# Optimization experiments

Hardware: AMD Instinct MI355X
Metric: run time of the kernel (lower is better)

## Reference

```python
import jax, jax.numpy as jnp
import numpy as np


def _conv(x, w, b=None, pad=0):
    y = jax.lax.conv_general_dilated(
        x, w, window_strides=(1, 1), padding=[(pad, pad), (pad, pad)],
        dimension_numbers=('NCHW', 'OIHW', 'NCHW'))
    if b is not None:
        y = y + b[None, :, None, None]
    return y


def _resblock(x, w1, w2):
    r = _conv(x, w1, pad=1)
    r = jnp.where(r > 0, r, 0.1 * r)  # LeakyReLU(0.1)
    r = _conv(r, w2, pad=1)
    return r + x


def setup_inputs() -> dict:
    key = jax.random.key(0)
    ks = jax.random.split(key, 8)
    b, c, h, w = 8, 64, 128, 320
    return {
        'x_left': jax.random.normal(ks[0], (b, c, h, w), jnp.float32),
        'x_right': jax.random.normal(ks[1], (b, c, h, w), jnp.float32),
        'rb_w1': jax.random.normal(ks[2], (c, c, 3, 3), jnp.float32) * 0.05,
        'rb_w2': jax.random.normal(ks[3], (c, c, 3, 3), jnp.float32) * 0.05,
        'wl': jax.random.normal(ks[4], (c, c, 1, 1), jnp.float32) * 0.1,
        'bl': jax.random.normal(ks[5], (c,), jnp.float32) * 0.01,
        'wr': jax.random.normal(ks[6], (c, c, 1, 1), jnp.float32) * 0.1,
        'br': jax.random.normal(ks[7], (c,), jnp.float32) * 0.01,
    }


def reference(x_left, x_right, rb_w1, rb_w2, wl, bl, wr, br):
    b, c, h, w = x_left.shape
    buf_l = _resblock(x_left, rb_w1, rb_w2)
    buf_r = _resblock(x_right, rb_w1, rb_w2)
    # 1x1 projections, then per-row attention along width
    F0 = _conv(buf_l, wl, bl).transpose(0, 2, 3, 1)   # (b,h,w,c)
    F1 = _conv(buf_r, wr, br).transpose(0, 2, 3, 1)   # (b,h,w,c)
    S = jnp.einsum('bhwc,bhvc->bhwv', F0, F1)          # (b,h,w,w)
    M_right_to_left = jax.nn.softmax(S, axis=-1)       # (b,h,w,w)
    M_left_to_right = jax.nn.softmax(jnp.swapaxes(S, -1, -2), axis=-1)
    # validity mask: column-sum > 0.1 (detached). skimage morphology (CPU-side) is
    # intentionally omitted; it is outside the GPU kernel scope.
    V = (jnp.sum(jax.lax.stop_gradient(M_left_to_right), axis=2) > 0.1)
    V = V.reshape(b, 1, h, w).astype(jnp.float32)
    # warp right features to left view
    xr = x_right.transpose(0, 2, 3, 1)                 # (b,h,w,c)
    out_f = jnp.einsum('bhwv,bhvc->bhwc', M_right_to_left, xr)
    out_f = out_f.transpose(0, 3, 1, 2)                # (b,c,h,w)
    return (out_f, V,
            (M_left_to_right.reshape(b * h, w, w),
             M_right_to_left.reshape(b * h, w, w)))
```

## Files before the change

kernel.cpp:

```cpp
#include <hip/hip_runtime.h>

#define BB 8
#define CC 64
#define HH 128
#define WW 320

#define N_OUTF (BB*CC*HH*WW)
#define N_V    (BB*HH*WW)
#define N_M    (BB*HH*WW*WW)
#define OFF_V    (N_OUTF)
#define OFF_ML2R (N_OUTF + N_V)
#define OFF_MR2L (OFF_ML2R + N_M)
#define OUT_TOTAL (OFF_MR2L + N_M)
#define WT_FLOATS ((4*36864 + 4*4096)/2)
#define NCL 20971520
#define INV512 (1.f/512.f)

typedef _Float16 half8 __attribute__((ext_vector_type(8)));
typedef _Float16 half4 __attribute__((ext_vector_type(4)));
typedef float f32x4 __attribute__((ext_vector_type(4)));

__global__ __launch_bounds__(256) void k_wt(
    const float* __restrict__ w1, const float* __restrict__ w2,
    const float* __restrict__ wl, const float* __restrict__ wr,
    _Float16* __restrict__ wB1h, _Float16* __restrict__ wB1l,
    _Float16* __restrict__ wB2h, _Float16* __restrict__ wB2l,
    _Float16* __restrict__ wl1h, _Float16* __restrict__ wl1l,
    _Float16* __restrict__ wr1h, _Float16* __restrict__ wr1l)
{
    int tid = blockIdx.x * 256 + threadIdx.x;
    int stride = gridDim.x * 256;
    for (int e = tid; e < 64*9*64; e += stride) {
        int co = e / 576;
        int rem = e - co*576;
        int tap = rem >> 6, ci = rem & 63;
        float v1 = w1[(co*64 + ci)*9 + tap];
        float v2 = w2[(co*64 + ci)*9 + tap];
        _Float16 h1 = (_Float16)v1, h2 = (_Float16)v2;
        wB1h[e] = h1; wB1l[e] = (_Float16)((v1 - (float)h1)*512.f);
        wB2h[e] = h2; wB2l[e] = (_Float16)((v2 - (float)h2)*512.f);
    }
    for (int e = tid; e < 4096; e += stride) {
        float vl = wl[e], vr = wr[e];
        _Float16 hl = (_Float16)vl, hr = (_Float16)vr;
        wl1h[e] = hl; wl1l[e] = (_Float16)((vl - (float)hl)*512.f);
        wr1h[e] = hr; wr1l[e] = (_Float16)((vr - (float)hr)*512.f);
    }
}

__global__ __launch_bounds__(256) void k_conv_a(
    const float* __restrict__ in_l_, const float* __restrict__ in_r_,
    const _Float16* __restrict__ wBh, const _Float16* __restrict__ wBl,
    _Float16* __restrict__ r_lh, _Float16* __restrict__ r_ll,
    _Float16* __restrict__ r_rh, _Float16* __restrict__ r_rl)
{
    __shared__ __align__(16) char smem[2*4*34*128];
    char* in_sh = smem;
    char* in_sl = smem + 17408;
    const int tid = threadIdx.x;
    const int x0 = blockIdx.x * 32;
    const int y0 = blockIdx.y * 2;
    const int z  = blockIdx.z;
    const int side = z >> 3, b = z & 7;
    const float* in = side ? in_r_ : in_l_;
    _Float16* out_h = side ? r_rh : r_lh;
    _Float16* out_l = side ? r_rl : r_ll;
    const int lane = tid & 63;
    const int xq = lane & 15, kq = lane >> 4;
    const int n = tid >> 6;

    half8 bwh[18], bwl[18];
    {
        const _Float16* wbh = &wBh[((size_t)(n*16 + xq)*9)*64 + kq*8];
        const _Float16* wbl = &wBl[((size_t)(n*16 + xq)*9)*64 + kq*8];
#pragma unroll
        for (int t = 0; t < 9; ++t)
#pragma unroll
            for (int c = 0; c < 2; ++c) {
                bwh[t*2 + c] = *(const half8*)&wbh[t*64 + c*32];
                bwl[t*2 + c] = *(const half8*)&wbl[t*64 + c*32];
            }
    }

    for (int e = tid; e < 1088; e += 256) {
        int t = e / 34;
        int xx = e - t*34;
        int ry = t >> 3, u = t & 7;
        int gy = y0 + ry - 1, gx = x0 + xx - 1;
        half8 hh, hl;
#pragma unroll
        for (int j = 0; j < 8; ++j) { hh[j] = (_Float16)0.f; hl[j] = (_Float16)0.f; }
        if ((unsigned)gy < (unsigned)HH && (unsigned)gx < (unsigned)WW) {
            const float* p = &in[((size_t)(b*CC + u*8)*HH + gy)*WW + gx];
#pragma unroll
            for (int j = 0; j < 8; ++j) {
                float v = p[(size_t)j*HH*WW];
                _Float16 h = (_Float16)v;
                hh[j] = h; hl[j] = (_Float16)((v - (float)h)*512.f);
            }
        }
        int off = ((ry*34 + xx)*8 + (u ^ (xx & 7)))*16;
        *(half8*)&in_sh[off] = hh;
        *(half8*)&in_sl[off] = hl;
    }
    __syncthreads();

    f32x4 accm[2][2], accc[2][2];
#pragma unroll
    for (int rr = 0; rr < 2; ++rr)
#pragma unroll
        for (int m = 0; m < 2; ++m) { accm[rr][m] = (f32x4)0.f; accc[rr][m] = (f32x4)0.f; }

#pragma unroll
    for (int rr = 0; rr < 2; ++rr) {
#pragma unroll
        for (int m = 0; m < 2; ++m) {
            const int xb = m*16 + xq;
#pragma unroll
            for (int t = 0; t < 9; ++t) {
                const int ry = t / 3, kx = t - ry*3;
                const int trow = rr + ry;
                const int xxx = xb + kx;
#pragma unroll
                for (int c = 0; c < 2; ++c) {
                    const int u = c*4 + kq;
                    int off = ((trow*34 + xxx)*8 + (u ^ (xxx & 7)))*16;
                    half8 ah = *(const half8*)&in_sh[off];
                    half8 al = *(const half8*)&in_sl[off];
                    accm[rr][m] = __builtin_amdgcn_mfma_f32_16x16x32_f16(
                        ah, bwh[t*2 + c], accm[rr][m], 0, 0, 0);
                    accc[rr][m] = __builtin_amdgcn_mfma_f32_16x16x32_f16(
                        al, bwh[t*2 + c], accc[rr][m], 0, 0, 0);
                    accc[rr][m] = __builtin_amdgcn_mfma_f32_16x16x32_f16(
                        ah, bwl[t*2 + c], accc[rr][m], 0, 0, 0);
                }
            }
        }
    }
    __syncthreads();

    char* out_sh = smem;
    char* out_sl = smem + 8192;
#pragma unroll
    for (int rr = 0; rr < 2; ++rr) {
#pragma unroll
        for (int m = 0; m < 2; ++m) {
#pragma unroll
            for (int r = 0; r < 4; ++r) {
                int x = m*16 + kq*4 + r;
                int co = n*16 + xq;
                float v = accm[rr][m][r] + accc[rr][m][r]*INV512;
                v = (v > 0.f) ? v : 0.1f*v;
                _Float16 vh = (_Float16)v;
                _Float16 vl = (_Float16)((v - (float)vh)*512.f);
                int boff = ((rr*32 + x)*8 + ((co >> 3) ^ (x & 7)))*16 + (co & 7)*2;
                *(_Float16*)&out_sh[boff] = vh;
                *(_Float16*)&out_sl[boff] = vl;
            }
        }
    }
    __syncthreads();

#pragma unroll
    for (int i = 0; i < 2; ++i) {
        int unit = tid + 256*i;
        int rr = unit >> 8, x = (unit >> 3) & 31, u = unit & 7;
        int loff = ((rr*32 + x)*8 + (u ^ (x & 7)))*16;
        size_t g = (((size_t)(b*HH + y0 + rr)*WW) + x0 + x)*64 + u*8;
        *(half8*)&out_h[g] = *(half8*)&out_sh[loff];
        *(half8*)&out_l[g] = *(half8*)&out_sl[loff];
    }
}

__global__ __launch_bounds__(256) void k_conv_b(
    const _Float16* __restrict__ r_lh, const _Float16* __restrict__ r_ll,
    const _Float16* __restrict__ r_rh, const _Float16* __restrict__ r_rl,
    const _Float16* __restrict__ wBh, const _Float16* __restrict__ wBl,
    const float* __restrict__ res_l, const float* __restrict__ res_r,
    const _Float16* __restrict__ wl1h, const _Float16* __restrict__ wl1l,
    const _Float16* __restrict__ wr1h, const _Float16* __restrict__ wr1l,
    const float* __restrict__ bias_l, const float* __restrict__ bias_r,
    _Float16* __restrict__ F0h, _Float16* __restrict__ F0l,
    _Float16* __restrict__ F1h, _Float16* __restrict__ F1l)
{
    __shared__ __align__(16) char smem[49152];
    char* in_sh = smem;
    char* in_sl = smem + 17408;
    const int tid = threadIdx.x;
    const int x0 = blockIdx.x * 32;
    const int y0 = blockIdx.y * 2;
    const int z  = blockIdx.z;
    const int side = z >> 3, b = z & 7;
    const _Float16* in_h = side ? r_rh : r_lh;
    const _Float16* in_l = side ? r_rl : r_ll;
    const float* res = side ? res_r : res_l;
    const _Float16* w1h = side ? wr1h : wl1h;
    const _Float16* w1l = side ? wr1l : wl1l;
    const float* bias = side ? bias_r : bias_l;
    _Float16* Fh = side ? F1h : F0h;
    _Float16* Fl = side ? F1l : F0l;
    const int lane = tid & 63;
    const int xq = lane & 15, kq = lane >> 4;
    const int n = tid >> 6;

    half8 bwh[18], bwl[18];
    {
        const _Float16* wbh = &wBh[((size_t)(n*16 + xq)*9)*64 + kq*8];
        const _Float16* wbl = &wBl[((size_t)(n*16 + xq)*9)*64 + kq*8];
#pragma unroll
        for (int t = 0; t < 9; ++t)
#pragma unroll
            for (int c = 0; c < 2; ++c) {
                bwh[t*2 + c] = *(const half8*)&wbh[t*64 + c*32];
                bwl[t*2 + c] = *(const half8*)&wbl[t*64 + c*32];
            }
    }

    for (int e = tid; e < 1088; e += 256) {
        int t = e / 34;
        int xx = e - t*34;
        int ry = t >> 3, u = t & 7;
        int gy = y0 + ry - 1, gx = x0 + xx - 1;
        uint4 vh = make_uint4(0u,0u,0u,0u), vl = make_uint4(0u,0u,0u,0u);
        if ((unsigned)gy < (unsigned)HH && (unsigned)gx < (unsigned)WW) {
            size_t g = (((size_t)(b*HH + gy)*WW) + gx)*64 + u*8;
            vh = *(const uint4*)&in_h[g];
            vl = *(const uint4*)&in_l[g];
        }
        int off = ((ry*34 + xx)*8 + (u ^ (xx & 7)))*16;
        *(uint4*)&in_sh[off] = vh;
        *(uint4*)&in_sl[off] = vl;
    }
    __syncthreads();

    f32x4 accm[2][2], accc[2][2];
#pragma unroll
    for (int rr = 0; rr < 2; ++rr)
#pragma unroll
        for (int m = 0; m < 2; ++m) { accm[rr][m] = (f32x4)0.f; accc[rr][m] = (f32x4)0.f; }

#pragma unroll
    for (int rr = 0; rr < 2; ++rr) {
#pragma unroll
        for (int m = 0; m < 2; ++m) {
            const int xb = m*16 + xq;
#pragma unroll
            for (int t = 0; t < 9; ++t) {
                const int ry = t / 3, kx = t - ry*3;
                const int trow = rr + ry;
                const int xxx = xb + kx;
#pragma unroll
                for (int c = 0; c < 2; ++c) {
                    const int u = c*4 + kq;
                    int off = ((trow*34 + xxx)*8 + (u ^ (xxx & 7)))*16;
                    half8 ah = *(const half8*)&in_sh[off];
                    half8 al = *(const half8*)&in_sl[off];
                    accm[rr][m] = __builtin_amdgcn_mfma_f32_16x16x32_f16(
                        ah, bwh[t*2 + c], accm[rr][m], 0, 0, 0);
                    accc[rr][m] = __builtin_amdgcn_mfma_f32_16x16x32_f16(
                        al, bwh[t*2 + c], accc[rr][m], 0, 0, 0);
                    accc[rr][m] = __builtin_amdgcn_mfma_f32_16x16x32_f16(
                        ah, bwl[t*2 + c], accc[rr][m], 0, 0, 0);
                }
            }
        }
    }
    __syncthreads();

    char* out_sh = smem;
    char* out_sl = smem + 8192;
    char* res_sh = smem + 16384;
    char* res_sl = smem + 24576;
    char* w_sh   = smem + 32768;
    char* w_sl   = smem + 40960;

#pragma unroll
    for (int i = 0; i < 2; ++i) {
        int e = tid + 256*i;
        int rr = e >> 8, x = (e >> 3) & 31, cu = e & 7;
        const float* p = &res[((size_t)(b*CC + cu*8)*HH + y0 + rr)*WW + x0 + x];
        half8 hh, hl;
#pragma unroll
        for (int j = 0; j < 8; ++j) {
            float v = p[(size_t)j*HH*WW];
            _Float16 h = (_Float16)v;
            hh[j] = h; hl[j] = (_Float16)((v - (float)h)*512.f);
        }
        int off = ((rr*32 + x)*8 + (cu ^ (x & 7)))*16;
        *(half8*)&res_sh[off] = hh;
        *(half8*)&res_sl[off] = hl;
    }
#pragma unroll
    for (int i = 0; i < 2; ++i) {
        int e = tid + 256*i;
        int co = e >> 3, u = e & 7;
        int off = (co*8 + (u ^ (co & 7)))*16;
        *(half8*)&w_sh[off] = *(const half8*)&w1h[co*64 + u*8];
        *(half8*)&w_sl[off] = *(const half8*)&w1l[co*64 + u*8];
    }
#pragma unroll
    for (int rr = 0; rr < 2; ++rr) {
#pragma unroll
        for (int m = 0; m < 2; ++m) {
#pragma unroll
            for (int r = 0; r < 4; ++r) {
                int x = m*16 + kq*4 + r;
                int co = n*16 + xq;
                float v = accm[rr][m][r] + accc[rr][m][r]*INV512;
                _Float16 vh = (_Float16)v;
                _Float16 vl = (_Float16)((v - (float)vh)*512.f);
                int boff = ((rr*32 + x)*8 + ((co >> 3) ^ (x & 7)))*16 + (co & 7)*2;
                *(_Float16*)&out_sh[boff] = vh;
                *(_Float16*)&out_sl[boff] = vl;
            }
        }
    }
    __syncthreads();

    float bv[4];
#pragma unroll
    for (int nn = 0; nn < 4; ++nn) bv[nn] = bias[nn*16 + (lane & 15)];

    f32x4 am[4], ac[4];
#pragma unroll
    for (int nn = 0; nn < 4; ++nn) { am[nn] = (f32x4)0.f; ac[nn] = (f32x4)0.f; }

    const int arow = n*16 + (lane & 15);
#pragma unroll
    for (int c = 0; c < 4; ++c) {
        half8 ah, al;
        int u = (c & 1)*4 + (lane >> 4);
        int off = (arow*8 + (u ^ (arow & 7)))*16;
        if (c < 2) {
            ah = *(const half8*)&out_sh[off];
            al = *(const half8*)&out_sl[off];
        } else {
            ah = *(const half8*)&res_sh[off];
            al = *(const half8*)&res_sl[off];
        }
#pragma unroll
        for (int nn = 0; nn < 4; ++nn) {
            int brow = nn*16 + (lane & 15);
            int woff = (brow*8 + (u ^ (brow & 7)))*16;
            half8 bh  = *(const half8*)&w_sh[woff];
            half8 blw = *(const half8*)&w_sl[woff];
            am[nn] = __builtin_amdgcn_mfma_f32_16x16x32_f16(ah, bh,  am[nn], 0,0,0);
            ac[nn] = __builtin_amdgcn_mfma_f32_16x16x32_f16(al, bh,  ac[nn], 0,0,0);
            ac[nn] = __builtin_amdgcn_mfma_f32_16x16x32_f16(ah, blw, ac[nn], 0,0,0);
        }
    }
    __syncthreads();

    char* F_sh = smem + 16384;
    char* F_sl = smem + 24576;
#pragma unroll
    for (int nn = 0; nn < 4; ++nn) {
#pragma unroll
        for (int r = 0; r < 4; ++r) {
            int pos = n*16 + (lane >> 4)*4 + r;
            int co = nn*16 + (lane & 15);
            float v = am[nn][r] + ac[nn][r]*INV512 + bv[nn];
            _Float16 vh = (_Float16)v;
            _Float16 vl = (_Float16)((v - (float)vh)*512.f);
            int boff = (pos*8 + ((co >> 3) ^ (pos & 7)))*16 + (co & 7)*2;
            *(_Float16*)&F_sh[boff] = vh;
            *(_Float16*)&F_sl[boff] = vl;
        }
    }
    __syncthreads();

#pragma unroll
    for (int i = 0; i < 2; ++i) {
        int unit = tid + 256*i;
        int rr = unit >> 8, x = (unit >> 3) & 31, u = unit & 7;
        int loff = ((rr*32 + x)*8 + (u ^ (x & 7)))*16;
        size_t g = (((size_t)(b*HH + y0 + rr)*WW) + x0 + x)*64 + u*8;
        *(half8*)&Fh[g] = *(half8*)&F_sh[loff];
        *(half8*)&Fl[g] = *(half8*)&F_sl[loff];
    }
}

__global__ __launch_bounds__(256) void k_sgemm(
    const _Float16* __restrict__ F0h, const _Float16* __restrict__ F0l,
    const _Float16* __restrict__ F1h, const _Float16* __restrict__ F1l,
    float* __restrict__ S,
    float* __restrict__ colmax_p, float* __restrict__ colsum_p,
    float* __restrict__ rowmax_f, float* __restrict__ rowinv_f)
{
    __shared__ __align__(16) char smem[32768];
    __shared__ float cpm[2][4][64], cpl[2][4][64];
    const int wt = blockIdx.x, row = blockIdx.y;
    const int tid = threadIdx.x, lane = tid & 63, wid = tid >> 6;
    char* R0 = smem;
    char* R1 = smem + 16384;

    for (int e = tid; e < 512; e += 256) {
        int i = e >> 3, u = e & 7;
        int off = (i*8 + (u ^ (i & 7)))*16;
        size_t ga = ((size_t)row*WW + wt*64 + i)*64 + u*8;
        *(uint4*)&R0[off]        = *(const uint4*)&F0h[ga];
        *(uint4*)&R0[8192 + off] = *(const uint4*)&F0l[ga];
        size_t gb = ((size_t)row*WW + i)*64 + u*8;
        *(uint4*)&R1[off]        = *(const uint4*)&F1h[gb];
        *(uint4*)&R1[8192 + off] = *(const uint4*)&F1l[gb];
    }
    __syncthreads();

    half8 ah[2], al[2];
    {
        const int arow = wid*16 + (lane & 15);
#pragma unroll
        for (int c = 0; c < 2; ++c) {
            int u = c*4 + (lane >> 4);
            int aoff = (arow*8 + (u ^ (arow & 7)))*16;
            ah[c] = *(const half8*)&R0[aoff];
            al[c] = *(const half8*)&R0[8192 + aoff];
        }
    }

    float rm[4], rl[4];
#pragma unroll
    for (int r = 0; r < 4; ++r) { rm[r] = -1e30f; rl[r] = 0.f; }

    for (int vt = 0; vt < 5; ++vt) {
        char* cur = (vt & 1) ? R0 : R1;
        __syncthreads();
        if (vt < 4) {
            char* nxt = (vt & 1) ? R1 : R0;
            for (int e = tid; e < 512; e += 256) {
                int i = e >> 3, u = e & 7;
                int off = (i*8 + (u ^ (i & 7)))*16;
                size_t gb = ((size_t)row*WW + (vt+1)*64 + i)*64 + u*8;
                *(uint4*)&nxt[off]        = *(const uint4*)&F1h[gb];
                *(uint4*)&nxt[8192 + off] = *(const uint4*)&F1l[gb];
            }
        }
        if (vt > 0 && tid < 64) {
            int pb = (vt-1) & 1;
            float m0 = cpm[pb][0][tid], m1 = cpm[pb][1][tid];
            float m2 = cpm[pb][2][tid], m3 = cpm[pb][3][tid];
            float m = fmaxf(fmaxf(m0, m1), fmaxf(m2, m3));
            float l = cpl[pb][0][tid]*__expf(m0-m) + cpl[pb][1][tid]*__expf(m1-m)
                    + cpl[pb][2][tid]*__expf(m2-m) + cpl[pb][3][tid]*__expf(m3-m);
            size_t cbase = ((size_t)row*5 + wt)*WW + (size_t)(vt-1)*64 + tid;
            colmax_p[cbase] = m;
            colsum_p[cbase] = l;
        }

        f32x4 accm[4], accc[4];
#pragma unroll
        for (int n = 0; n < 4; ++n) { accm[n] = (f32x4)0.f; accc[n] = (f32x4)0.f; }
#pragma unroll
        for (int c = 0; c < 2; ++c) {
            const int u = c*4 + (lane >> 4);
#pragma unroll
            for (int n = 0; n < 4; ++n) {
                const int brow = n*16 + (lane & 15);
                int boff = (brow*8 + (u ^ (brow & 7)))*16;
                half8 bh = *(const half8*)&cur[boff];
                half8 bl = *(const half8*)&cur[8192 + boff];
                accm[n] = __builtin_amdgcn_mfma_f32_16x16x32_f16(ah[c], bh, accm[n], 0,0,0);
                accc[n] = __builtin_amdgcn_mfma_f32_16x16x32_f16(al[c], bh, accc[n], 0,0,0);
                accc[n] = __builtin_amdgcn_mfma_f32_16x16x32_f16(ah[c], bl, accc[n], 0,0,0);
            }
        }

        float sv[4][4];
#pragma unroll
        for (int n = 0; n < 4; ++n)
#pragma unroll
            for (int r = 0; r < 4; ++r)
                sv[n][r] = accm[n][r] + accc[n][r]*INV512;

#pragma unroll
        for (int n = 0; n < 4; ++n) {
            float* sp = &S[((size_t)row*WW + wt*64 + wid*16 + (lane>>4)*4)*WW
                           + vt*64 + n*16 + (lane & 15)];
#pragma unroll
            for (int r = 0; r < 4; ++r) sp[(size_t)r*WW] = sv[n][r];
        }

#pragma unroll
        for (int r = 0; r < 4; ++r) {
            float tmax = fmaxf(fmaxf(sv[0][r], sv[1][r]), fmaxf(sv[2][r], sv[3][r]));
            float newm = fmaxf(rm[r], tmax);
            rl[r] = rl[r]*__expf(rm[r] - newm)
                  + __expf(sv[0][r]-newm) + __expf(sv[1][r]-newm)
                  + __expf(sv[2][r]-newm) + __expf(sv[3][r]-newm);
            rm[r] = newm;
        }

#pragma unroll
        for (int n = 0; n < 4; ++n) {
            float m = fmaxf(fmaxf(sv[n][0], sv[n][1]), fmaxf(sv[n][2], sv[n][3]));
            m = fmaxf(m, __shfl_xor(m, 16));
            m = fmaxf(m, __shfl_xor(m, 32));
            float l = __expf(sv[n][0]-m) + __expf(sv[n][1]-m)
                    + __expf(sv[n][2]-m) + __expf(sv[n][3]-m);
            l += __shfl_xor(l, 16); l += __shfl_xor(l, 32);
            if (lane < 16) { cpm[vt&1][wid][n*16 + lane] = m;
                             cpl[vt&1][wid][n*16 + lane] = l; }
        }
    }
    __syncthreads();
    if (tid < 64) {
        float m0 = cpm[0][0][tid], m1 = cpm[0][1][tid];
        float m2 = cpm[0][2][tid], m3 = cpm[0][3][tid];
        float m = fmaxf(fmaxf(m0, m1), fmaxf(m2, m3));
        float l = cpl[0][0][tid]*__expf(m0-m) + cpl[0][1][tid]*__expf(m1-m)
                + cpl[0][2][tid]*__expf(m2-m) + cpl[0][3][tid]*__expf(m3-m);
        size_t cbase = ((size_t)row*5 + wt)*WW + 4*64 + tid;
        colmax_p[cbase] = m;
        colsum_p[cbase] = l;
    }

#pragma unroll
    for (int r = 0; r < 4; ++r) {
#pragma unroll
        for (int o = 1; o < 16; o <<= 1) {
            float m2 = __shfl_xor(rm[r], o);
            float l2 = __shfl_xor(rl[r], o);
            float mm = fmaxf(rm[r], m2);
            rl[r] = rl[r]*__expf(rm[r] - mm) + l2*__expf(m2 - mm);
            rm[r] = mm;
        }
    }
    if ((lane & 15) == 0) {
        size_t rbase = (size_t)row*WW + wt*64 + wid*16 + (lane>>4)*4;
#pragma unroll
        for (int r = 0; r < 4; ++r) {
            rowmax_f[rbase + r] = rm[r];
            rowinv_f[rbase + r] = 1.f / rl[r];
        }
    }
}

__global__ __launch_bounds__(320) void k_smerge(
    const float* __restrict__ colmax_p, const float* __restrict__ colsum_p,
    float* __restrict__ colmax_f, float* __restrict__ colinv_f)
{
    const int row = blockIdx.x, tid = threadIdx.x;
    float m = -1e30f, l = 0.f;
#pragma unroll
    for (int t = 0; t < 5; ++t) {
        float pm = colmax_p[((size_t)row*5 + t)*WW + tid];
        float pl = colsum_p[((size_t)row*5 + t)*WW + tid];
        float m2 = fmaxf(m, pm);
        l = l*__expf(m - m2) + pl*__expf(pm - m2);
        m = m2;
    }
    colmax_f[(size_t)row*WW + tid] = m;
    colinv_f[(size_t)row*WW + tid] = 1.f/l;
}

__global__ __launch_bounds__(256) void k_fused(
    float* __restrict__ S, float* __restrict__ Ml2r, float* __restrict__ Vout,
    const float* __restrict__ xr, float* __restrict__ outf,
    const float* __restrict__ colmax_f, const float* __restrict__ colinv_f,
    const float* __restrict__ rowmax_f, const float* __restrict__ rowinv_f)
{
    __shared__ __align__(16) char A[8192], Bm[8192];
    __shared__ float T[64*65];
    __shared__ float cmx[320], cin[320], rmx[64], rin[64];
    const int wt = blockIdx.x, row = blockIdx.y;
    const int b = row >> 7, h = row & 127;
    const int tid = threadIdx.x, lane = tid & 63, wid = tid >> 6;
    const int wrow = tid >> 2, quad = tid & 3;

    for (int e = tid; e < 320; e += 256) {
        cmx[e] = colmax_f[(size_t)row*WW + e];
        cin[e] = colinv_f[(size_t)row*WW + e];
    }
    if (tid < 64) {
        rmx[tid] = rowmax_f[(size_t)row*WW + wt*64 + tid];
        rin[tid] = rowinv_f[(size_t)row*WW + wt*64 + tid];
    }
    __syncthreads();

    f32x4 acc[4];
#pragma unroll
    for (int n = 0; n < 4; ++n) acc[n] = (f32x4)0.f;
    float vsum = 0.f;
    float* Sbase = &S[((size_t)row*WW + wt*64 + wrow)*WW];
    const float rm = rmx[wrow], ri = rin[wrow];

    float4 s_pre[4];
#pragma unroll
    for (int i = 0; i < 4; ++i)
        s_pre[i] = *(float4*)&Sbase[(quad + 4*i)*4];

    for (int vt = 0; vt < 5; ++vt) {
        if (vt) __syncthreads();
        float4 s_cur[4];
#pragma unroll
        for (int i = 0; i < 4; ++i) s_cur[i] = s_pre[i];
        if (vt < 4) {
#pragma unroll
            for (int i = 0; i < 4; ++i)
                s_pre[i] = *(float4*)&Sbase[(vt+1)*64 + (quad + 4*i)*4];
        }
#pragma unroll
        for (int i = 0; i < 4; ++i) {
            const int f = quad + 4*i;
            const int v0 = f*4;
            float4 s = s_cur[i];
            float4 pr;
            pr.x = __expf(s.x - rm)*ri;
            pr.y = __expf(s.y - rm)*ri;
            pr.z = __expf(s.z - rm)*ri;
            pr.w = __expf(s.w - rm)*ri;
            *(float4*)&Sbase[vt*64 + v0] = pr;
            const int vg = vt*64 + v0;
            float p0 = __expf(s.x - cmx[vg+0])*cin[vg+0];
            float p1 = __expf(s.y - cmx[vg+1])*cin[vg+1];
            float p2 = __expf(s.z - cmx[vg+2])*cin[vg+2];
            float p3 = __expf(s.w - cmx[vg+3])*cin[vg+3];
            T[(v0+0)*65 + wrow] = p0;
            T[(v0+1)*65 + wrow] = p1;
            T[(v0+2)*65 + wrow] = p2;
            T[(v0+3)*65 + wrow] = p3;
            vsum += p0 + p1 + p2 + p3;
            half4 hp;
            hp[0] = (_Float16)pr.x; hp[1] = (_Float16)pr.y;
            hp[2] = (_Float16)pr.z; hp[3] = (_Float16)pr.w;
            *(half4*)&A[(wrow*8 + ((f>>1) ^ (wrow & 7)))*16 + (f & 1)*8] = hp;
        }
        for (int e = tid; e < 512; e += 256) {
            int i = e >> 3, u = e & 7;
            const float4* xp = (const float4*)
                &xr[(((size_t)b*CC + i)*HH + h)*WW + vt*64 + u*8];
            float4 b0 = xp[0], b1 = xp[1];
            half8 hb;
            hb[0]=(_Float16)b0.x; hb[1]=(_Float16)b0.y; hb[2]=(_Float16)b0.z;
            hb[3]=(_Float16)b0.w; hb[4]=(_Float16)b1.x; hb[5]=(_Float16)b1.y;
            hb[6]=(_Float16)b1.z; hb[7]=(_Float16)b1.w;
            *(half8*)&Bm[(i*8 + (u ^ (i & 7)))*16] = hb;
        }
        __syncthreads();
#pragma unroll
        for (int c = 0; c < 2; ++c) {
            const int u = c*4 + (lane >> 4);
            const int arow = wid*16 + (lane & 15);
            half8 ah = *(const half8*)&A[(arow*8 + (u ^ (arow & 7)))*16];
#pragma unroll
            for (int n = 0; n < 4; ++n) {
                const int brow = n*16 + (lane & 15);
                half8 bh = *(const half8*)&Bm[(brow*8 + (u ^ (brow & 7)))*16];
                acc[n] = __builtin_amdgcn_mfma_f32_16x16x32_f16(ah, bh, acc[n], 0,0,0);
            }
        }
        for (int e = tid; e < 1024; e += 256) {
            int vr = e >> 4, wc4 = (e & 15)*4;
            const float* tp = &T[vr*65 + wc4];
            *(float4*)&Ml2r[((size_t)row*WW + vt*64 + vr)*WW + wt*64 + wc4] =
                make_float4(tp[0], tp[1], tp[2], tp[3]);
        }
    }

    vsum += __shfl_xor(vsum, 1);
    vsum += __shfl_xor(vsum, 2);
    if (quad == 0)
        Vout[(size_t)row*WW + wt*64 + wrow] = (vsum > 0.1f) ? 1.f : 0.f;

#pragma unroll
    for (int n = 0; n < 4; ++n) {
        *(float4*)&outf[(((size_t)b*CC + n*16 + (lane & 15))*HH + h)*WW
                        + wt*64 + wid*16 + (lane>>4)*4] =
            make_float4(acc[n][0], acc[n][1], acc[n][2], acc[n][3]);
    }
}

__global__ __launch_bounds__(320) void k_softmax(
    float* __restrict__ S, float* __restrict__ Ml2r, float* __restrict__ Vout,
    const float* __restrict__ colmax_f, const float* __restrict__ colinv_f,
    const float* __restrict__ rowmax_f, const float* __restrict__ rowinv_f)
{
    __shared__ float rowmax[320], rowinv[320], colmax[320], colinv[320];
    __shared__ float T[64*65];
    __shared__ float Vp2[5*64];
    const int row = blockIdx.x;
    const int tid = threadIdx.x;
    float* Srow = &S[(size_t)row * WW * WW];

    rowmax[tid] = rowmax_f[(size_t)row*WW + tid];
    rowinv[tid] = rowinv_f[(size_t)row*WW + tid];
    colmax[tid] = colmax_f[(size_t)row*WW + tid];
    colinv[tid] = colinv_f[(size_t)row*WW + tid];
    __syncthreads();

    const int myw = tid & 63;
    const int myg = tid / 64;
    for (int wt = 0; wt < 5; ++wt) {
        float vpart = 0.f;
        for (int vt = 0; vt < 5; ++vt) {
            for (int e = tid; e < 4096; e += 320) {
                int i = e >> 6, j = e & 63;
                int wgl = wt*64 + i, vgl = vt*64 + j;
                size_t si = (size_t)wgl*WW + vgl;
                float s = Srow[si];
                Srow[si] = __expf(s - rowmax[wgl]) * rowinv[wgl];
                T[j*65 + i] = __expf(s - colmax[vgl]) * colinv[vgl];
            }
            __syncthreads();
            for (int e = tid; e < 4096; e += 320) {
                int vr = e >> 6, wc = e & 63;
                Ml2r[((size_t)row*WW + vt*64 + vr)*WW + wt*64 + wc] = T[vr*65 + wc];
            }
            for (int j = myg; j < 64; j += 5) vpart += T[j*65 + myw];
            __syncthreads();
        }
        Vp2[myg*64 + myw] = vpart;
        __syncthreads();
        if (tid < 64) {
            float sv = 0.f;
#pragma unroll
            for (int g = 0; g < 5; ++g) sv += Vp2[g*64 + tid];
            Vout[(size_t)row*WW + wt*64 + tid] = (sv > 0.1f) ? 1.f : 0.f;
        }
        __syncthreads();
    }
}

__global__ __launch_bounds__(256) void k_outgemm(
    const float* __restrict__ M, const float* __restrict__ xr,
    float* __restrict__ outf)
{
    __shared__ __align__(16) char Am[8192], Bm[8192];
    const int wt = blockIdx.x;
    const int row = blockIdx.y;
    const int b = row >> 7, h = row & 127;
    const int tid = threadIdx.x, lane = tid & 63, wid = tid >> 6;

    f32x4 acc[4];
#pragma unroll
    for (int n = 0; n < 4; ++n) acc[n] = (f32x4)0.f;

    for (int vt = 0; vt < 5; ++vt) {
        if (vt) __syncthreads();
        for (int e = tid; e < 512; e += 256) {
            int i = e >> 3, u = e & 7;
            const float4* mp = (const float4*)
                &M[((size_t)row*WW + wt*64 + i)*WW + vt*64 + u*8];
            float4 a0 = mp[0], a1 = mp[1];
            const float4* xp = (const float4*)
                &xr[(((size_t)b*CC + i)*HH + h)*WW + vt*64 + u*8];
            float4 b0 = xp[0], b1 = xp[1];
            half8 ha, hb;
            ha[0]=(_Float16)a0.x; ha[1]=(_Float16)a0.y; ha[2]=(_Float16)a0.z;
            ha[3]=(_Float16)a0.w; ha[4]=(_Float16)a1.x; ha[5]=(_Float16)a1.y;
            ha[6]=(_Float16)a1.z; ha[7]=(_Float16)a1.w;
            hb[0]=(_Float16)b0.x; hb[1]=(_Float16)b0.y; hb[2]=(_Float16)b0.z;
            hb[3]=(_Float16)b0.w; hb[4]=(_Float16)b1.x; hb[5]=(_Float16)b1.y;
            hb[6]=(_Float16)b1.z; hb[7]=(_Float16)b1.w;
            int off = (i*8 + (u ^ (i & 7)))*16;
            *(half8*)&Am[off] = ha;
            *(half8*)&Bm[off] = hb;
        }
        __syncthreads();
#pragma unroll
        for (int c = 0; c < 2; ++c) {
            const int u = c*4 + (lane >> 4);
            const int arow = wid*16 + (lane & 15);
            half8 ah = *(const half8*)&Am[(arow*8 + (u ^ (arow & 7)))*16];
#pragma unroll
            for (int n = 0; n < 4; ++n) {
                const int brow = n*16 + (lane & 15);
                half8 bh = *(const half8*)&Bm[(brow*8 + (u ^ (brow & 7)))*16];
                acc[n] = __builtin_amdgcn_mfma_f32_16x16x32_f16(ah, bh, acc[n], 0,0,0);
            }
        }
    }

#pragma unroll
    for (int n = 0; n < 4; ++n) {
        *(float4*)&outf[(((size_t)b*CC + n*16 + (lane & 15))*HH + h)*WW
                        + wt*64 + wid*16 + (lane>>4)*4] =
            make_float4(acc[n][0], acc[n][1], acc[n][2], acc[n][3]);
    }
}

extern "C" void kernel_launch(void* const* d_in, const int* in_sizes, int n_in,
                              void* d_out, int out_size, void* d_ws, size_t ws_size,
                              hipStream_t stream)
{
    const float* x_l = (const float*)d_in[0];
    const float* x_r = (const float*)d_in[1];
    const float* w1  = (const float*)d_in[2];
    const float* w2  = (const float*)d_in[3];
    const float* wl  = (const float*)d_in[4];
    const float* bl  = (const float*)d_in[5];
    const float* wr  = (const float*)d_in[6];
    const float* br  = (const float*)d_in[7];
    float* out = (float*)d_out;

    float* outf = out;
    float* Vp   = out + OFF_V;
    float* Ml2r = out + OFF_ML2R;
    float* Mr2l = out + OFF_MR2L;

    _Float16* r_lh = (_Float16*)Mr2l;
    _Float16* r_ll = r_lh + 1*(size_t)NCL;
    _Float16* r_rh = r_lh + 2*(size_t)NCL;
    _Float16* r_rl = r_lh + 3*(size_t)NCL;
    _Float16* F0h = (_Float16*)Ml2r;
    _Float16* F0l = F0h + (size_t)NCL;
    _Float16* F1h = F0l + (size_t)NCL;
    _Float16* F1l = F1h + (size_t)NCL;
    float* S  = Mr2l;
    _Float16* WTH = (_Float16*)(Ml2r + (size_t)N_M - WT_FLOATS);
    _Float16* wB1h = WTH;
    _Float16* wB1l = WTH + 36864;
    _Float16* wB2h = WTH + 73728;
    _Float16* wB2l = WTH + 110592;
    _Float16* wl1h = WTH + 147456;
    _Float16* wl1l = WTH + 151552;
    _Float16* wr1h = WTH + 155648;
    _Float16* wr1l = WTH + 159744;
    float* colmax_p = out + 0;
    float* colsum_p = out + 1700000;

    const size_t FIN_FLOATS = (size_t)1024*320;
    bool fused = ws_size >= 4*FIN_FLOATS*sizeof(float);
    float* colmax_f, *colinv_f, *rowmax_f, *rowinv_f;
    if (fused) {
        float* ws = (float*)d_ws;
        colmax_f = ws + 0*FIN_FLOATS;
        colinv_f = ws + 1*FIN_FLOATS;
        rowmax_f = ws + 2*FIN_FLOATS;
        rowinv_f = ws + 3*FIN_FLOATS;
    } else {
        colmax_f = out + 6800000;
        colinv_f = out + 7200000;
        rowmax_f = out + 7600000;
        rowinv_f = out + 8000000;
    }

    k_wt<<<64, 256, 0, stream>>>(w1, w2, wl, wr,
                                 wB1h, wB1l, wB2h, wB2l,
                                 wl1h, wl1l, wr1h, wr1l);

    dim3 pgrid(WW/32, HH/2, BB*2);
    k_conv_a<<<pgrid, 256, 0, stream>>>(x_l, x_r, wB1h, wB1l,
                                        r_lh, r_ll, r_rh, r_rl);
    k_conv_b<<<pgrid, 256, 0, stream>>>(r_lh, r_ll, r_rh, r_rl,
                                        wB2h, wB2l, x_l, x_r,
                                        wl1h, wl1l, wr1h, wr1l, bl, br,
                                        F0h, F0l, F1h, F1l);

    dim3 sgrid(5, BB*HH);
    k_sgemm<<<sgrid, 256, 0, stream>>>(F0h, F0l, F1h, F1l, S,
                                       colmax_p, colsum_p,
                                       rowmax_f, rowinv_f);

    k_smerge<<<BB*HH, 320, 0, stream>>>(colmax_p, colsum_p,
                                        colmax_f, colinv_f);

    if (fused) {
        dim3 fgrid(5, BB*HH);
        k_fused<<<fgrid, 256, 0, stream>>>(S, Ml2r, Vp, x_r, outf,
                                           colmax_f, colinv_f,
                                           rowmax_f, rowinv_f);
    } else {
        k_softmax<<<BB*HH, 320, 0, stream>>>(S, Ml2r, Vp,
                                             colmax_f, colinv_f,
                                             rowmax_f, rowinv_f);
        dim3 ogrid(5, BB*HH);
        k_outgemm<<<ogrid, 256, 0, stream>>>(Mr2l, x_r, outf);
    }
}
```

Before: 1.117 ms.

## Recompute scores in fused softmax kernel instead of storing and rereading S

When the workspace is large enough, the F0/F1 half-precision features move into the workspace so the score matrix no longer has to live in the output buffer. The stats pass skips writing S, and a new fused kernel recomputes S per tile with MFMA. From the recomputed S it then writes both softmax outputs, the validity mask and the warped features. This removes a full write and read of the large fp32 score tensor at the cost of running the score GEMM twice. The old non-workspace fallback kernels are removed, so without workspace the older fused path runs.

```diff
diff --git a/kernel.cpp b/kernel.cpp
--- a/kernel.cpp
+++ b/kernel.cpp
@@ -380,6 +380,7 @@
     }
 }
 
+template<bool WRITE_S>
 __global__ __launch_bounds__(256) void k_sgemm(
     const _Float16* __restrict__ F0h, const _Float16* __restrict__ F0l,
     const _Float16* __restrict__ F1h, const _Float16* __restrict__ F1l,
@@ -472,12 +473,14 @@
             for (int r = 0; r < 4; ++r)
                 sv[n][r] = accm[n][r] + accc[n][r]*INV512;
 
-#pragma unroll
-        for (int n = 0; n < 4; ++n) {
-            float* sp = &S[((size_t)row*WW + wt*64 + wid*16 + (lane>>4)*4)*WW
-                           + vt*64 + n*16 + (lane & 15)];
-#pragma unroll
-            for (int r = 0; r < 4; ++r) sp[(size_t)r*WW] = sv[n][r];
+        if (WRITE_S) {
+#pragma unroll
+            for (int n = 0; n < 4; ++n) {
+                float* sp = &S[((size_t)row*WW + wt*64 + wid*16 + (lane>>4)*4)*WW
+                               + vt*64 + n*16 + (lane & 15)];
+#pragma unroll
+                for (int r = 0; r < 4; ++r) sp[(size_t)r*WW] = sv[n][r];
+            }
         }
 
 #pragma unroll
@@ -551,6 +554,163 @@
     }
     colmax_f[(size_t)row*WW + tid] = m;
     colinv_f[(size_t)row*WW + tid] = 1.f/l;
+}
+
+__global__ __launch_bounds__(256) void k_fused2(
+    const _Float16* __restrict__ F0h, const _Float16* __restrict__ F0l,
+    const _Float16* __restrict__ F1h, const _Float16* __restrict__ F1l,
+    float* __restrict__ Ml2r, float* __restrict__ Mr2l,
+    float* __restrict__ Vout,
+    const float* __restrict__ xr, float* __restrict__ outf,
+    const float* __restrict__ colmax_f, const float* __restrict__ colinv_f,
+    const float* __restrict__ rowmax_f, const float* __restrict__ rowinv_f)
+{
+    __shared__ __align__(16) char smem[65536];
+    char* A_sh = smem;
+    char* A_sl = smem + 8192;
+    char* B_sh = smem + 16384;
+    char* B_sl = smem + 24576;
+    float* T   = (float*)(smem + 32768);
+    char* Am   = smem + 49152;
+    char* Bm   = smem + 57344;
+    const int wt = blockIdx.x, row = blockIdx.y;
+    const int b = row >> 7, h = row & 127;
+    const int tid = threadIdx.x, lane = tid & 63, wid = tid >> 6;
+
+    for (int e = tid; e < 512; e += 256) {
+        int i = e >> 3, u = e & 7;
+        int off = (i*8 + (u ^ (i & 7)))*16;
+        size_t ga = ((size_t)row*WW + wt*64 + i)*64 + u*8;
+        *(uint4*)&A_sh[off] = *(const uint4*)&F0h[ga];
+        *(uint4*)&A_sl[off] = *(const uint4*)&F0l[ga];
+    }
+    const int w_lo = wid*16 + (lane >> 4)*4;
+    float rmv[4], riv[4];
+#pragma unroll
+    for (int r = 0; r < 4; ++r) {
+        rmv[r] = rowmax_f[(size_t)row*WW + wt*64 + w_lo + r];
+        riv[r] = rowinv_f[(size_t)row*WW + wt*64 + w_lo + r];
+    }
+    __syncthreads();
+
+    half8 ah[2], al[2];
+    {
+        const int arow = wid*16 + (lane & 15);
+#pragma unroll
+        for (int c = 0; c < 2; ++c) {
+            int u = c*4 + (lane >> 4);
+            int aoff = (arow*8 + (u ^ (arow & 7)))*16;
+            ah[c] = *(const half8*)&A_sh[aoff];
+            al[c] = *(const half8*)&A_sl[aoff];
+        }
+    }
+
+    f32x4 acc[4];
+#pragma unroll
+    for (int n = 0; n < 4; ++n) acc[n] = (f32x4)0.f;
+    float vsum[4] = {0.f, 0.f, 0.f, 0.f};
+
+    for (int vt = 0; vt < 5; ++vt) {
+        if (vt) __syncthreads();
+        for (int e = tid; e < 512; e += 256) {
+            int i = e >> 3, u = e & 7;
+            int off = (i*8 + (u ^ (i & 7)))*16;
+            size_t gb = ((size_t)row*WW + vt*64 + i)*64 + u*8;
+            *(uint4*)&B_sh[off] = *(const uint4*)&F1h[gb];
+            *(uint4*)&B_sl[off] = *(const uint4*)&F1l[gb];
+            const float4* xp = (const float4*)
+                &xr[(((size_t)b*CC + i)*HH + h)*WW + vt*64 + u*8];
+            float4 b0 = xp[0], b1 = xp[1];
+            half8 hb;
+            hb[0]=(_Float16)b0.x; hb[1]=(_Float16)b0.y; hb[2]=(_Float16)b0.z;
+            hb[3]=(_Float16)b0.w; hb[4]=(_Float16)b1.x; hb[5]=(_Float16)b1.y;
+            hb[6]=(_Float16)b1.z; hb[7]=(_Float16)b1.w;
+            *(half8*)&Bm[off] = hb;
+        }
+        float cmv[4], civ[4];
+#pragma unroll
+        for (int n = 0; n < 4; ++n) {
+            size_t vg = (size_t)row*WW + vt*64 + n*16 + (lane & 15);
+            cmv[n] = colmax_f[vg];
+            civ[n] = colinv_f[vg];
+        }
+        __syncthreads();
+
+        f32x4 sm[4], sc[4];
+#pragma unroll
+        for (int n = 0; n < 4; ++n) { sm[n] = (f32x4)0.f; sc[n] = (f32x4)0.f; }
+#pragma unroll
+        for (int c = 0; c < 2; ++c) {
+            const int u = c*4 + (lane >> 4);
+#pragma unroll
+            for (int n = 0; n < 4; ++n) {
+                const int brow = n*16 + (lane & 15);
+                int boff = (brow*8 + (u ^ (brow & 7)))*16;
+                half8 bh = *(const half8*)&B_sh[boff];
+                half8 bl = *(const half8*)&B_sl[boff];
+                sm[n] = __builtin_amdgcn_mfma_f32_16x16x32_f16(ah[c], bh, sm[n], 0,0,0);
+                sc[n] = __builtin_amdgcn_mfma_f32_16x16x32_f16(al[c], bh, sc[n], 0,0,0);
+                sc[n] = __builtin_amdgcn_mfma_f32_16x16x32_f16(ah[c], bl, sc[n], 0,0,0);
+            }
+        }
+
+#pragma unroll
+        for (int n = 0; n < 4; ++n) {
+            const int v = n*16 + (lane & 15);
+            float* mp = &Mr2l[((size_t)row*WW + wt*64 + w_lo)*WW + vt*64 + v];
+#pragma unroll
+            for (int r = 0; r < 4; ++r) {
+                float s = sm[n][r] + sc[n][r]*INV512;
+                float pr = __expf(s - rmv[r])*riv[r];
+                float pc = __expf(s - cmv[n])*civ[n];
+                mp[(size_t)r*WW] = pr;
+                T[v*64 + ((w_lo + r) ^ ((v & 7) << 2))] = pc;
+                vsum[r] += pc;
+                int w = w_lo + r;
+                *(_Float16*)&Am[(w*8 + ((v >> 3) ^ (w & 7)))*16 + (v & 7)*2]
+                    = (_Float16)pr;
+            }
+        }
+        __syncthreads();
+
+#pragma unroll
+        for (int c = 0; c < 2; ++c) {
+            const int u = c*4 + (lane >> 4);
+            const int arow = wid*16 + (lane & 15);
+            half8 ap = *(const half8*)&Am[(arow*8 + (u ^ (arow & 7)))*16];
+#pragma unroll
+            for (int n = 0; n < 4; ++n) {
+                const int brow = n*16 + (lane & 15);
+                half8 bh = *(const half8*)&Bm[(brow*8 + (u ^ (brow & 7)))*16];
+                acc[n] = __builtin_amdgcn_mfma_f32_16x16x32_f16(ap, bh, acc[n], 0,0,0);
+            }
+        }
+        for (int e = tid; e < 1024; e += 256) {
+            int vr = e >> 4, wc4 = (e & 15)*4;
+            const float* tp = &T[vr*64 + (wc4 ^ ((vr & 7) << 2))];
+            *(float4*)&Ml2r[((size_t)row*WW + vt*64 + vr)*WW + wt*64 + wc4] =
+                make_float4(tp[0], tp[1], tp[2], tp[3]);
+        }
+    }
+
+#pragma unroll
+    for (int r = 0; r < 4; ++r) {
+#pragma unroll
+        for (int o = 1; o < 16; o <<= 1)
+            vsum[r] += __shfl_xor(vsum[r], o);
+    }
+    if ((lane & 15) == 0) {
+#pragma unroll
+        for (int r = 0; r < 4; ++r)
+            Vout[(size_t)row*WW + wt*64 + w_lo + r] = (vsum[r] > 0.1f) ? 1.f : 0.f;
+    }
+
+#pragma unroll
+    for (int n = 0; n < 4; ++n) {
+        *(float4*)&outf[(((size_t)b*CC + n*16 + (lane & 15))*HH + h)*WW
+                        + wt*64 + wid*16 + (lane>>4)*4] =
+            make_float4(acc[n][0], acc[n][1], acc[n][2], acc[n][3]);
+    }
 }
 
 __global__ __launch_bounds__(256) void k_fused(
@@ -670,115 +830,6 @@
     }
 }
 
-__global__ __launch_bounds__(320) void k_softmax(
-    float* __restrict__ S, float* __restrict__ Ml2r, float* __restrict__ Vout,
-    const float* __restrict__ colmax_f, const float* __restrict__ colinv_f,
-    const float* __restrict__ rowmax_f, const float* __restrict__ rowinv_f)
-{
-    __shared__ float rowmax[320], rowinv[320], colmax[320], colinv[320];
-    __shared__ float T[64*65];
-    __shared__ float Vp2[5*64];
-    const int row = blockIdx.x;
-    const int tid = threadIdx.x;
-    float* Srow = &S[(size_t)row * WW * WW];
-
-    rowmax[tid] = rowmax_f[(size_t)row*WW + tid];
-    rowinv[tid] = rowinv_f[(size_t)row*WW + tid];
-    colmax[tid] = colmax_f[(size_t)row*WW + tid];
-    colinv[tid] = colinv_f[(size_t)row*WW + tid];
-    __syncthreads();
-
-    const int myw = tid & 63;
-    const int myg = tid / 64;
-    for (int wt = 0; wt < 5; ++wt) {
-        float vpart = 0.f;
-        for (int vt = 0; vt < 5; ++vt) {
-            for (int e = tid; e < 4096; e += 320) {
-                int i = e >> 6, j = e & 63;
-                int wgl = wt*64 + i, vgl = vt*64 + j;
-                size_t si = (size_t)wgl*WW + vgl;
-                float s = Srow[si];
-                Srow[si] = __expf(s - rowmax[wgl]) * rowinv[wgl];
-                T[j*65 + i] = __expf(s - colmax[vgl]) * colinv[vgl];
-            }
-            __syncthreads();
-            for (int e = tid; e < 4096; e += 320) {
-                int vr = e >> 6, wc = e & 63;
-                Ml2r[((size_t)row*WW + vt*64 + vr)*WW + wt*64 + wc] = T[vr*65 + wc];
-            }
-            for (int j = myg; j < 64; j += 5) vpart += T[j*65 + myw];
-            __syncthreads();
-        }
-        Vp2[myg*64 + myw] = vpart;
-        __syncthreads();
-        if (tid < 64) {
-            float sv = 0.f;
-#pragma unroll
-            for (int g = 0; g < 5; ++g) sv += Vp2[g*64 + tid];
-            Vout[(size_t)row*WW + wt*64 + tid] = (sv > 0.1f) ? 1.f : 0.f;
-        }
-        __syncthreads();
-    }
-}
-
-__global__ __launch_bounds__(256) void k_outgemm(
-    const float* __restrict__ M, const float* __restrict__ xr,
-    float* __restrict__ outf)
-{
-    __shared__ __align__(16) char Am[8192], Bm[8192];
-    const int wt = blockIdx.x;
-    const int row = blockIdx.y;
-    const int b = row >> 7, h = row & 127;
-    const int tid = threadIdx.x, lane = tid & 63, wid = tid >> 6;
-
-    f32x4 acc[4];
-#pragma unroll
-    for (int n = 0; n < 4; ++n) acc[n] = (f32x4)0.f;
-
-    for (int vt = 0; vt < 5; ++vt) {
-        if (vt) __syncthreads();
-        for (int e = tid; e < 512; e += 256) {
-            int i = e >> 3, u = e & 7;
-            const float4* mp = (const float4*)
-                &M[((size_t)row*WW + wt*64 + i)*WW + vt*64 + u*8];
-            float4 a0 = mp[0], a1 = mp[1];
-            const float4* xp = (const float4*)
-                &xr[(((size_t)b*CC + i)*HH + h)*WW + vt*64 + u*8];
-            float4 b0 = xp[0], b1 = xp[1];
-            half8 ha, hb;
-            ha[0]=(_Float16)a0.x; ha[1]=(_Float16)a0.y; ha[2]=(_Float16)a0.z;
-            ha[3]=(_Float16)a0.w; ha[4]=(_Float16)a1.x; ha[5]=(_Float16)a1.y;
-            ha[6]=(_Float16)a1.z; ha[7]=(_Float16)a1.w;
-            hb[0]=(_Float16)b0.x; hb[1]=(_Float16)b0.y; hb[2]=(_Float16)b0.z;
-            hb[3]=(_Float16)b0.w; hb[4]=(_Float16)b1.x; hb[5]=(_Float16)b1.y;
-            hb[6]=(_Float16)b1.z; hb[7]=(_Float16)b1.w;
-            int off = (i*8 + (u ^ (i & 7)))*16;
-            *(half8*)&Am[off] = ha;
-            *(half8*)&Bm[off] = hb;
-        }
-        __syncthreads();
-#pragma unroll
-        for (int c = 0; c < 2; ++c) {
-            const int u = c*4 + (lane >> 4);
-            const int arow = wid*16 + (lane & 15);
-            half8 ah = *(const half8*)&Am[(arow*8 + (u ^ (arow & 7)))*16];
-#pragma unroll
-            for (int n = 0; n < 4; ++n) {
-                const int brow = n*16 + (lane & 15);
-                half8 bh = *(const half8*)&Bm[(brow*8 + (u ^ (brow & 7)))*16];
-                acc[n] = __builtin_amdgcn_mfma_f32_16x16x32_f16(ah, bh, acc[n], 0,0,0);
-            }
-        }
-    }
-
-#pragma unroll
-    for (int n = 0; n < 4; ++n) {
-        *(float4*)&outf[(((size_t)b*CC + n*16 + (lane & 15))*HH + h)*WW
-                        + wt*64 + wid*16 + (lane>>4)*4] =
-            make_float4(acc[n][0], acc[n][1], acc[n][2], acc[n][3]);
-    }
-}
-
 extern "C" void kernel_launch(void* const* d_in, const int* in_sizes, int n_in,
                               void* d_out, int out_size, void* d_ws, size_t ws_size,
                               hipStream_t stream)
@@ -802,10 +853,6 @@
     _Float16* r_ll = r_lh + 1*(size_t)NCL;
     _Float16* r_rh = r_lh + 2*(size_t)NCL;
     _Float16* r_rl = r_lh + 3*(size_t)NCL;
-    _Float16* F0h = (_Float16*)Ml2r;
-    _Float16* F0l = F0h + (size_t)NCL;
-    _Float16* F1h = F0l + (size_t)NCL;
-    _Float16* F1l = F1h + (size_t)NCL;
     float* S  = Mr2l;
     _Float16* WTH = (_Float16*)(Ml2r + (size_t)N_M - WT_FLOATS);
     _Float16* wB1h = WTH;
@@ -820,9 +867,13 @@
     float* colsum_p = out + 1700000;
 
     const size_t FIN_FLOATS = (size_t)1024*320;
-    bool fused = ws_size >= 4*FIN_FLOATS*sizeof(float);
-    float* colmax_f, *colinv_f, *rowmax_f, *rowinv_f;
-    if (fused) {
+    const size_t NCLF = (size_t)NCL/2;
+    bool noS = ws_size >= (4*FIN_FLOATS + 4*NCLF)*sizeof(float);
+    bool fusedOK = ws_size >= 4*FIN_FLOATS*sizeof(float);
+
+    float *colmax_f, *colinv_f, *rowmax_f, *rowinv_f;
+    _Float16 *F0h, *F0l, *F1h, *F1l;
+    if (fusedOK) {
         float* ws = (float*)d_ws;
         colmax_f = ws + 0*FIN_FLOATS;
         colinv_f = ws + 1*FIN_FLOATS;
@@ -834,6 +885,18 @@
         rowmax_f = out + 7600000;
         rowinv_f = out + 8000000;
     }
+    if (noS) {
+        _Float16* wsF = (_Float16*)((float*)d_ws + 4*FIN_FLOATS);
+        F0h = wsF;
+        F0l = F0h + (size_t)NCL;
+        F1h = F0l + (size_t)NCL;
+        F1l = F1h + (size_t)NCL;
+    } else {
+        F0h = (_Float16*)Ml2r;
+        F0l = F0h + (size_t)NCL;
+        F1h = F0l + (size_t)NCL;
+        F1l = F1h + (size_t)NCL;
+    }
 
     k_wt<<<64, 256, 0, stream>>>(w1, w2, wl, wr,
                                  wB1h, wB1l, wB2h, wB2l,
@@ -848,23 +911,28 @@
                                         F0h, F0l, F1h, F1l);
 
     dim3 sgrid(5, BB*HH);
-    k_sgemm<<<sgrid, 256, 0, stream>>>(F0h, F0l, F1h, F1l, S,
-                                       colmax_p, colsum_p,
-                                       rowmax_f, rowinv_f);
+    if (noS) {
+        k_sgemm<false><<<sgrid, 256, 0, stream>>>(F0h, F0l, F1h, F1l, S,
+                                                  colmax_p, colsum_p,
+                                                  rowmax_f, rowinv_f);
+    } else {
+        k_sgemm<true><<<sgrid, 256, 0, stream>>>(F0h, F0l, F1h, F1l, S,
+                                                 colmax_p, colsum_p,
+                                                 rowmax_f, rowinv_f);
+    }
 
     k_smerge<<<BB*HH, 320, 0, stream>>>(colmax_p, colsum_p,
                                         colmax_f, colinv_f);
 
-    if (fused) {
-        dim3 fgrid(5, BB*HH);
+    dim3 fgrid(5, BB*HH);
+    if (noS) {
+        k_fused2<<<fgrid, 256, 0, stream>>>(F0h, F0l, F1h, F1l,
+                                            Ml2r, Mr2l, Vp, x_r, outf,
+                                            colmax_f, colinv_f,
+                                            rowmax_f, rowinv_f);
+    } else {
         k_fused<<<fgrid, 256, 0, stream>>>(S, Ml2r, Vp, x_r, outf,
                                            colmax_f, colinv_f,
                                            rowmax_f, rowinv_f);
-    } else {
-        k_softmax<<<BB*HH, 320, 0, stream>>>(S, Ml2r, Vp,
-                                             colmax_f, colinv_f,
-                                             rowmax_f, rowinv_f);
-        dim3 ogrid(5, BB*HH);
-        k_outgemm<<<ogrid, 256, 0, stream>>>(Mr2l, x_r, outf);
     }
 }
```

After: 1.095 ms. Within noise of the previous version (-1.9%).
